# Optimization experiments

Measured on AMD Instinct MI355X. Metric: run time of the kernel, lower is better.

## Reference

```python
import jax, jax.numpy as jnp
import numpy as np

HIDDEN = 2048
INTER = 768
N_EXPERTS = 8
TOP_K = 2
BATCH, SEQ = 4, 512


def setup_inputs() -> dict:
    key = jax.random.key(0)
    ks = jax.random.split(key, 5)
    std = 0.02
    hidden_states = jax.random.normal(ks[0], (BATCH, SEQ, HIDDEN), dtype=jnp.float32)
    W_gate = jax.random.normal(ks[1], (N_EXPERTS, HIDDEN), dtype=jnp.float32) * std  # router Linear weight [E,H]
    Wg = jax.random.normal(ks[2], (N_EXPERTS, HIDDEN, INTER), dtype=jnp.float32) * std  # gate proj per expert
    Wu = jax.random.normal(ks[3], (N_EXPERTS, HIDDEN, INTER), dtype=jnp.float32) * std  # up proj per expert
    Wd = jax.random.normal(ks[4], (N_EXPERTS, INTER, HIDDEN), dtype=jnp.float32) * std  # down proj per expert
    return {"hidden_states": hidden_states, "W_gate": W_gate, "Wg": Wg, "Wu": Wu, "Wd": Wd}


def reference(hidden_states, W_gate, Wg, Wu, Wd):
    orig_shape = hidden_states.shape
    x = hidden_states.reshape(-1, HIDDEN)              # [T, H]
    T = x.shape[0]

    # Router: softmax in float32, top-k, renormalize (matches torch code).
    router_logits = x @ W_gate.T                        # [T, E]
    routing_probs = jax.nn.softmax(router_logits.astype(jnp.float32), axis=-1)
    topk_w, topk_idx = jax.lax.top_k(routing_probs, TOP_K)  # [T, K]
    topk_w = topk_w / jnp.sum(topk_w, axis=-1, keepdims=True)
    topk_w = topk_w.astype(x.dtype)

    # Sparse combine weights as dense [T, E] (equiv to index_add over torch.where dispatch).
    combine = jnp.zeros((T, N_EXPERTS), dtype=x.dtype)
    combine = combine.at[jnp.arange(T)[:, None], topk_idx].add(topk_w)

    # Expert MLPs, computed densely over experts (idiomatic jit-able dispatch).
    g = jnp.einsum('th,ehi->eti', x, Wg)                # [E, T, I]
    u = jnp.einsum('th,ehi->eti', x, Wu)                # [E, T, I]
    h = jax.nn.silu(g) * u                              # SiluAndMul
    y = jnp.einsum('eti,eih->eth', h, Wd)               # [E, T, H]

    out = jnp.einsum('eth,te->th', y, combine)          # weighted combine
    return out.reshape(orig_shape)
```

## Files before the change

### kernel.cpp

```cpp
#include <hip/hip_runtime.h>
#include <hip/hip_bf16.h>
#include <math.h>

#define H_DIM 2048
#define I_DIM 768
#define NEXP  8
#define TTOK  2048

typedef __bf16 bf16x8 __attribute__((ext_vector_type(8)));
typedef __bf16 bf16x4 __attribute__((ext_vector_type(4)));
typedef float  f32x4  __attribute__((ext_vector_type(4)));

#define WS_COUNTS   0u
#define WS_TOK      128u
#define WS_WGTW     65664u
#define WS_XBF      131328u
#define WS_HBUF     8519936u
#define WS_WG_T     15008000u
#define WS_WU_T     40173824u
#define WS_WD_T     65339648u


__device__ __forceinline__ void gl2l(const __bf16* g, __bf16* l) {
    __builtin_amdgcn_global_load_lds(
        (const __attribute__((address_space(1))) unsigned int*)g,
        (__attribute__((address_space(3))) unsigned int*)l, 16, 0, 0);
}

__device__ __forceinline__ void pipe_sync_vm8() {
    asm volatile("" ::: "memory");
    __builtin_amdgcn_s_waitcnt(0x78);
    __builtin_amdgcn_s_barrier();
    asm volatile("" ::: "memory");
}
__device__ __forceinline__ void pipe_sync_vm4() {
    asm volatile("" ::: "memory");
    __builtin_amdgcn_s_waitcnt(0x74);
    __builtin_amdgcn_s_barrier();
    asm volatile("" ::: "memory");
}
__device__ __forceinline__ void pipe_sync_vm0() {
    asm volatile("" ::: "memory");
    __builtin_amdgcn_s_waitcnt(0x70);
    __builtin_amdgcn_s_barrier();
    asm volatile("" ::: "memory");
}

#define NTRANS 18432
__global__ __launch_bounds__(128) void prep_k(
    const float* __restrict__ x, const float* __restrict__ Wgate,
    const float* __restrict__ Wg, const float* __restrict__ Wu, const float* __restrict__ Wd,
    int* __restrict__ counts, int* __restrict__ tok_list, float* __restrict__ wgt,
    __bf16* __restrict__ xb, __bf16* __restrict__ Wg_t, __bf16* __restrict__ Wu_t,
    __bf16* __restrict__ Wd_t) {
    __shared__ float sT[64 * 33];
    __shared__ float s_red[NEXP][2];
    __shared__ float s_logit[NEXP];
    const int tid = threadIdx.x;
    const int b = blockIdx.x;

    if (b >= NTRANS) {
        const int t = b - NTRANS;
        const float4* xr = (const float4*)(x + (size_t)t * H_DIM);
        bf16x4* xo = (bf16x4*)(xb + (size_t)t * H_DIM);
        float acc[NEXP];
#pragma unroll
        for (int e = 0; e < NEXP; ++e) acc[e] = 0.f;
#pragma unroll
        for (int j = 0; j < 4; ++j) {
            const int i4 = j * 128 + tid;
            float4 v = xr[i4];
            bf16x4 o;
            o[0] = (__bf16)v.x; o[1] = (__bf16)v.y; o[2] = (__bf16)v.z; o[3] = (__bf16)v.w;
            xo[i4] = o;
#pragma unroll
            for (int e = 0; e < NEXP; ++e) {
                float4 wv = *(const float4*)(Wgate + e * H_DIM + i4 * 4);
                acc[e] += v.x * wv.x + v.y * wv.y + v.z * wv.z + v.w * wv.w;
            }
        }
        const int lane = tid & 63, w = tid >> 6;
#pragma unroll
        for (int e = 0; e < NEXP; ++e) {
            float v = acc[e];
#pragma unroll
            for (int off = 32; off > 0; off >>= 1) v += __shfl_down(v, off, 64);
            if (lane == 0) s_red[e][w] = v;
        }
        __syncthreads();
        if (tid < NEXP) s_logit[tid] = s_red[tid][0] + s_red[tid][1];
        __syncthreads();
        if (tid == 0) {
            int i0 = 0; float l0 = s_logit[0];
            for (int e = 1; e < NEXP; ++e) if (s_logit[e] > l0) { l0 = s_logit[e]; i0 = e; }
            int i1 = -1; float l1 = -1e30f;
            for (int e = 0; e < NEXP; ++e) if (e != i0 && s_logit[e] > l1) { l1 = s_logit[e]; i1 = e; }
            float w0 = 1.f / (1.f + expf(l1 - l0));
            float w1 = 1.f - w0;
            int p0 = atomicAdd(&counts[i0], 1);
            tok_list[i0 * TTOK + p0] = t; wgt[i0 * TTOK + p0] = w0;
            int p1 = atomicAdd(&counts[i1], 1);
            tok_list[i1 * TTOK + p1] = t; wgt[i1 * TTOK + p1] = w1;
        }
        return;
    }

    int r = b;
    const int t3 = r / 6144; r -= t3 * 6144;
    const int e = r / 768;  const int rem = r - e * 768;
    const float* in; __bf16* out; int N, k0, n0;
    size_t tbase; int rowbase;
    if (t3 < 2) {
        N = I_DIM;
        const int kt = rem / 12, nt = rem % 12;
        k0 = kt * 32; n0 = nt * 64;
        in = t3 ? Wu : Wg; out = t3 ? Wu_t : Wg_t;
        tbase = ((size_t)(e * 12 + nt) * 64 + kt) * 2048;
        rowbase = 0;
    } else {
        N = H_DIM;
        const int kt = rem / 32, ntraw = rem % 32;
        k0 = kt * 32; n0 = ntraw * 64;
        in = Wd; out = Wd_t;
        tbase = ((size_t)(e * 16 + (ntraw >> 1)) * 24 + kt) * 4096;
        rowbase = (ntraw & 1) * 64;
    }
    const float* ip = in + (size_t)e * (N == I_DIM ? H_DIM * I_DIM : I_DIM * H_DIM);
    const int kl = tid >> 4;
    const int n4 = (tid & 15) * 4;
#pragma unroll
    for (int j = 0; j < 4; ++j) {
        int k = kl + j * 8;
        float4 v = *(const float4*)(ip + (size_t)(k0 + k) * N + n0 + n4);
        sT[(n4 + 0) * 33 + k] = v.x;
        sT[(n4 + 1) * 33 + k] = v.y;
        sT[(n4 + 2) * 33 + k] = v.z;
        sT[(n4 + 3) * 33 + k] = v.w;
    }
    __syncthreads();
    const int rn = tid >> 1;
    const int c0 = (tid & 1) * 2;
    bf16x8 o0, o1;
#pragma unroll
    for (int j = 0; j < 8; ++j) {
        o0[j] = (__bf16)sT[rn * 33 + c0 * 8 + j];
        o1[j] = (__bf16)sT[rn * 33 + c0 * 8 + 8 + j];
    }
    const int s0 = c0 ^ (rn & 3), s1 = s0 ^ 1;
    __bf16* op = out + tbase + (size_t)(rowbase + rn) * 32;
    *(bf16x8*)(op + s0 * 8) = o0;
    *(bf16x8*)(op + s1 * 8) = o1;
}

__global__ __launch_bounds__(256, 2) void gemm1_k(
    const __bf16* __restrict__ xb, const __bf16* __restrict__ Wgt,
    const __bf16* __restrict__ Wut, const int* __restrict__ counts,
    const int* __restrict__ tok_list, __bf16* __restrict__ hbuf) {
    const int g = blockIdx.x;
    const int e = g / 12, nt = g % 12;
    const int cnt = counts[e];
    const int m0 = blockIdx.y * 128;
    if (m0 >= cnt) return;
    const int tid = threadIdx.x;
    const int lane = tid & 63, w = tid >> 6;

    __shared__ __bf16 sA[4][128 * 32];
    __shared__ __bf16 sG_[4][64 * 32];
    __shared__ __bf16 sU[4][64 * 32];
    __shared__ int s_tok[128];
    __shared__ int s_off;

    if (tid == 0) { int o = 0; for (int j = 0; j < e; ++j) o += counts[j]; s_off = o; }
    if (tid < 128) {
        int m = m0 + tid;
        s_tok[tid] = tok_list[e * TTOK + (m < cnt ? m : cnt - 1)];
    }
    __syncthreads();
    const int off = s_off;

    const int srow = lane >> 2;
    const int gof = ((lane & 3) ^ (srow & 3)) * 8;
    const __bf16* pA[2]; int lofA[2];
#pragma unroll
    for (int i = 0; i < 2; ++i) {
        int r = i * 64 + w * 16 + srow;
        pA[i] = xb + (size_t)s_tok[r] * H_DIM + gof;
        lofA[i] = (i * 64 + w * 16) * 32;
    }
    const int lofGU = (w * 16) * 32;
    const __bf16* pG = Wgt + (size_t)(e * 12 + nt) * 64 * 2048 + w * 512 + lane * 8;
    const __bf16* pU = Wut + (size_t)(e * 12 + nt) * 64 * 2048 + w * 512 + lane * 8;

    const int wm = w & 1, wn = w >> 1;
    const int l15 = lane & 15, kq = lane >> 4;
    const int swz = (kq ^ (l15 & 3)) * 8;

    f32x4 accG[4][2], accU[4][2];
#pragma unroll
    for (int mf = 0; mf < 4; ++mf)
#pragma unroll
        for (int nf = 0; nf < 2; ++nf) {
            accG[mf][nf] = (f32x4){0.f, 0.f, 0.f, 0.f};
            accU[mf][nf] = (f32x4){0.f, 0.f, 0.f, 0.f};
        }

#define G1_ISSUE(T, BUF)                                             \
    {                                                                \
        gl2l(pA[0] + (T) * 32, &sA[BUF][lofA[0]]);                   \
        gl2l(pA[1] + (T) * 32, &sA[BUF][lofA[1]]);                   \
        gl2l(pG + (T) * 2048, &sG_[BUF][lofGU]);                     \
        gl2l(pU + (T) * 2048, &sU[BUF][lofGU]);                      \
    }

#define G1_COMPUTE(P)                                                                    \
    {                                                                                    \
        bf16x8 af[4], bg[2], bu[2];                                                      \
        _Pragma("unroll")                                                                \
        for (int mf = 0; mf < 4; ++mf)                                                   \
            af[mf] = *(const bf16x8*)(&sA[P][0] + (wm * 64 + mf * 16 + l15) * 32 + swz); \
        _Pragma("unroll")                                                                \
        for (int nf = 0; nf < 2; ++nf) {                                                 \
            bg[nf] = *(const bf16x8*)(&sG_[P][0] + (wn * 32 + nf * 16 + l15) * 32 + swz);\
            bu[nf] = *(const bf16x8*)(&sU[P][0] + (wn * 32 + nf * 16 + l15) * 32 + swz); \
        }                                                                                \
        _Pragma("unroll")                                                                \
        for (int mf = 0; mf < 4; ++mf)                                                   \
            _Pragma("unroll")                                                            \
            for (int nf = 0; nf < 2; ++nf) {                                             \
                accG[mf][nf] = __builtin_amdgcn_mfma_f32_16x16x32_bf16(af[mf], bg[nf], accG[mf][nf], 0, 0, 0); \
                accU[mf][nf] = __builtin_amdgcn_mfma_f32_16x16x32_bf16(af[mf], bu[nf], accU[mf][nf], 0, 0, 0); \
            }                                                                            \
    }

    G1_ISSUE(0, 0); G1_ISSUE(1, 1); G1_ISSUE(2, 2);

#pragma unroll 4
    for (int it = 0; it < 60; ++it) {
        const int p = it & 3;
        pipe_sync_vm8();
        G1_ISSUE(it + 3, (it + 3) & 3);
        G1_COMPUTE(p);
    }
    pipe_sync_vm8(); G1_ISSUE(63, 3); G1_COMPUTE(0);
    pipe_sync_vm8(); G1_COMPUTE(1);
    pipe_sync_vm4(); G1_COMPUTE(2);
    pipe_sync_vm0(); G1_COMPUTE(3);
#undef G1_ISSUE
#undef G1_COMPUTE

#pragma unroll
    for (int mf = 0; mf < 4; ++mf) {
#pragma unroll
        for (int reg = 0; reg < 4; ++reg) {
            int m = m0 + wm * 64 + mf * 16 + kq * 4 + reg;
            if (m < cnt) {
                size_t rowbase = (size_t)(off + m) * I_DIM;
#pragma unroll
                for (int nf = 0; nf < 2; ++nf) {
                    float g1 = accG[mf][nf][reg], u1 = accU[mf][nf][reg];
                    float h = (g1 / (1.f + __expf(-g1))) * u1;
                    hbuf[rowbase + nt * 64 + wn * 32 + nf * 16 + l15] = (__bf16)h;
                }
            }
        }
    }
}

__global__ __launch_bounds__(256, 2) void gemm2_k(
    const __bf16* __restrict__ hbuf, const __bf16* __restrict__ Wdt,
    const int* __restrict__ counts, const int* __restrict__ tok_list,
    const float* __restrict__ wgt, float* __restrict__ out) {
    const int g = blockIdx.x;
    const int e = g >> 4, nt = g & 15;
    const int cnt = counts[e];
    const int m0 = blockIdx.y * 128;
    if (m0 >= cnt) return;
    const int tid = threadIdx.x;
    const int lane = tid & 63, w = tid >> 6;

    __shared__ __bf16 sA[4][128 * 32];
    __shared__ __bf16 sB[4][128 * 32];
    __shared__ int s_tok[128];
    __shared__ float s_w[128];
    __shared__ int s_off;

    if (tid == 0) { int o = 0; for (int j = 0; j < e; ++j) o += counts[j]; s_off = o; }
    if (tid < 128) {
        int m = m0 + tid;
        if (m < cnt) { s_tok[tid] = tok_list[e * TTOK + m]; s_w[tid] = wgt[e * TTOK + m]; }
        else         { s_tok[tid] = 0;                      s_w[tid] = 0.f; }
    }
    __syncthreads();
    const int off = s_off;

    const int srow = lane >> 2;
    const int gof = ((lane & 3) ^ (srow & 3)) * 8;
    const __bf16* pA[2]; int lofA[2];
#pragma unroll
    for (int i = 0; i < 2; ++i) {
        int r = i * 64 + w * 16 + srow;
        pA[i] = hbuf + (size_t)(off + m0 + r) * I_DIM + gof;
        lofA[i] = (i * 64 + w * 16) * 32;
    }
    const int lofB0 = (w * 16) * 32;
    const int lofB1 = (64 + w * 16) * 32;
    const __bf16* pB0 = Wdt + (size_t)(e * 16 + nt) * 24 * 4096 + (w * 16) * 32 + lane * 8;
    const __bf16* pB1 = pB0 + 64 * 32;

    const int wm = w & 1, wn = w >> 1;
    const int l15 = lane & 15, kq = lane >> 4;
    const int swz = (kq ^ (l15 & 3)) * 8;

    f32x4 acc[4][4];
#pragma unroll
    for (int mf = 0; mf < 4; ++mf)
#pragma unroll
        for (int nf = 0; nf < 4; ++nf) acc[mf][nf] = (f32x4){0.f, 0.f, 0.f, 0.f};

#define G2_ISSUE(T, BUF)                                             \
    {                                                                \
        gl2l(pA[0] + (T) * 32, &sA[BUF][lofA[0]]);                   \
        gl2l(pA[1] + (T) * 32, &sA[BUF][lofA[1]]);                   \
        gl2l(pB0 + (T) * 4096, &sB[BUF][lofB0]);                     \
        gl2l(pB1 + (T) * 4096, &sB[BUF][lofB1]);                     \
    }

#define G2_COMPUTE(P)                                                                    \
    {                                                                                    \
        bf16x8 af[4], bb[4];                                                             \
        _Pragma("unroll")                                                                \
        for (int mf = 0; mf < 4; ++mf)                                                   \
            af[mf] = *(const bf16x8*)(&sA[P][0] + (wm * 64 + mf * 16 + l15) * 32 + swz); \
        _Pragma("unroll")                                                                \
        for (int nf = 0; nf < 4; ++nf)                                                   \
            bb[nf] = *(const bf16x8*)(&sB[P][0] + (wn * 64 + nf * 16 + l15) * 32 + swz); \
        _Pragma("unroll")                                                                \
        for (int mf = 0; mf < 4; ++mf)                                                   \
            _Pragma("unroll")                                                            \
            for (int nf = 0; nf < 4; ++nf)                                               \
                acc[mf][nf] = __builtin_amdgcn_mfma_f32_16x16x32_bf16(af[mf], bb[nf], acc[mf][nf], 0, 0, 0); \
    }

    G2_ISSUE(0, 0); G2_ISSUE(1, 1); G2_ISSUE(2, 2);
#pragma unroll 4
    for (int it = 0; it < 20; ++it) {
        const int p = it & 3;
        pipe_sync_vm8();
        G2_ISSUE(it + 3, (it + 3) & 3);
        G2_COMPUTE(p);
    }
    pipe_sync_vm8(); G2_ISSUE(23, 3); G2_COMPUTE(0);
    pipe_sync_vm8(); G2_COMPUTE(1);
    pipe_sync_vm4(); G2_COMPUTE(2);
    pipe_sync_vm0(); G2_COMPUTE(3);
#undef G2_ISSUE
#undef G2_COMPUTE

#pragma unroll
    for (int mf = 0; mf < 4; ++mf) {
#pragma unroll
        for (int reg = 0; reg < 4; ++reg) {
            int m_loc = wm * 64 + mf * 16 + kq * 4 + reg;
            if (m0 + m_loc < cnt) {
                int tok = s_tok[m_loc];
                float wv = s_w[m_loc];
                float* orow = out + (size_t)tok * H_DIM + nt * 128 + wn * 64 + l15;
#pragma unroll
                for (int nf = 0; nf < 4; ++nf)
                    atomicAdd(orow + nf * 16, wv * acc[mf][nf][reg]);
            }
        }
    }
}

extern "C" void kernel_launch(void* const* d_in, const int* in_sizes, int n_in,
                              void* d_out, int out_size, void* d_ws, size_t ws_size,
                              hipStream_t stream) {
    const float* x     = (const float*)d_in[0];
    const float* Wgate = (const float*)d_in[1];
    const float* Wg    = (const float*)d_in[2];
    const float* Wu    = (const float*)d_in[3];
    const float* Wd    = (const float*)d_in[4];
    float* out = (float*)d_out;
    char* ws = (char*)d_ws;

    int*    counts   = (int*)(ws + WS_COUNTS);
    int*    tok_list = (int*)(ws + WS_TOK);
    float*  wgt      = (float*)(ws + WS_WGTW);
    __bf16* xb       = (__bf16*)(ws + WS_XBF);
    __bf16* hbuf     = (__bf16*)(ws + WS_HBUF);
    __bf16* Wg_t     = (__bf16*)(ws + WS_WG_T);
    __bf16* Wu_t     = (__bf16*)(ws + WS_WU_T);
    __bf16* Wd_t     = (__bf16*)(ws + WS_WD_T);

    hipMemsetAsync(counts, 0, 32, stream);
    hipMemsetAsync(d_out, 0, (size_t)TTOK * H_DIM * sizeof(float), stream);

    prep_k<<<NTRANS + TTOK, 128, 0, stream>>>(x, Wgate, Wg, Wu, Wd,
                                              counts, tok_list, wgt, xb, Wg_t, Wu_t, Wd_t);
    gemm1_k<<<dim3(96, 16), 256, 0, stream>>>(xb, Wg_t, Wu_t, counts, tok_list, hbuf);
    gemm2_k<<<dim3(128, 16), 256, 0, stream>>>(hbuf, Wd_t, counts, tok_list, wgt, out);
}
```

Measured before the change: 340.4 us.

## Restructure weight transpose prep into large coalesced row-strip blocks

The weight conversion/transpose kernel now gives each 256-thread block a full 32-row strip. That strip covers all 768 columns for Wg/Wu, or 512 columns for Wd. Rows are read with fully contiguous float4 loads, converted to bf16 in shared memory, then written out as swizzled 32-wide tiles. This replaces 18432 small 128-thread blocks with 1792 larger blocks, aiming to improve DRAM read coalescing and cut per-block overhead in the memory-bound prep stage. The router blocks move to 256 threads with a 4-wave reduction; larger shared memory per block may lower occupancy.

Measured after the change: 346.8 us. No clear change (+1.9%).

```diff
diff --git a/kernel.cpp b/kernel.cpp
--- a/kernel.cpp
+++ b/kernel.cpp
@@ -46,110 +46,136 @@
     asm volatile("" ::: "memory");
 }
 
-#define NTRANS 18432
-__global__ __launch_bounds__(128) void prep_k(
+#define NBLK_A  1024
+#define NBLK_AB 1792
+__global__ __launch_bounds__(256) void prep_k(
     const float* __restrict__ x, const float* __restrict__ Wgate,
     const float* __restrict__ Wg, const float* __restrict__ Wu, const float* __restrict__ Wd,
     int* __restrict__ counts, int* __restrict__ tok_list, float* __restrict__ wgt,
     __bf16* __restrict__ xb, __bf16* __restrict__ Wg_t, __bf16* __restrict__ Wu_t,
     __bf16* __restrict__ Wd_t) {
-    __shared__ float sT[64 * 33];
-    __shared__ float s_red[NEXP][2];
+    __shared__ __bf16 sTb[32 * 772];
+    __shared__ float s_red[NEXP][4];
     __shared__ float s_logit[NEXP];
     const int tid = threadIdx.x;
     const int b = blockIdx.x;
 
-    if (b >= NTRANS) {
-        const int t = b - NTRANS;
-        const float4* xr = (const float4*)(x + (size_t)t * H_DIM);
-        bf16x4* xo = (bf16x4*)(xb + (size_t)t * H_DIM);
-        float acc[NEXP];
-#pragma unroll
-        for (int e = 0; e < NEXP; ++e) acc[e] = 0.f;
-#pragma unroll
-        for (int j = 0; j < 4; ++j) {
-            const int i4 = j * 128 + tid;
-            float4 v = xr[i4];
+    if (b < NBLK_A) {
+        const int which = b >> 9;
+        const int e = (b >> 6) & 7;
+        const int kt = b & 63;
+        const float4* ip4 = (const float4*)((which ? Wu : Wg) + ((size_t)e * H_DIM + kt * 32) * I_DIM);
+#pragma unroll
+        for (int i = 0; i < 24; ++i) {
+            const int f = i * 256 + tid;
+            const int k = f / 192;
+            const int n4 = (f - k * 192) * 4;
+            float4 v = ip4[f];
             bf16x4 o;
             o[0] = (__bf16)v.x; o[1] = (__bf16)v.y; o[2] = (__bf16)v.z; o[3] = (__bf16)v.w;
-            xo[i4] = o;
-#pragma unroll
-            for (int e = 0; e < NEXP; ++e) {
-                float4 wv = *(const float4*)(Wgate + e * H_DIM + i4 * 4);
-                acc[e] += v.x * wv.x + v.y * wv.y + v.z * wv.z + v.w * wv.w;
+            *(bf16x4*)(&sTb[k * 772 + n4]) = o;
+        }
+        __syncthreads();
+        __bf16* outp = which ? Wu_t : Wg_t;
+#pragma unroll
+        for (int i = 0; i < 3; ++i) {
+            const int n = i * 256 + tid;
+            const int nt = n >> 6, rn = n & 63;
+            __bf16 col[32];
+#pragma unroll
+            for (int k = 0; k < 32; ++k) col[k] = sTb[k * 772 + n];
+            __bf16* op = outp + ((size_t)((e * 12 + nt) * 64 + kt)) * 2048 + rn * 32;
+            const int sw = rn & 3;
+#pragma unroll
+            for (int c = 0; c < 4; ++c) {
+                bf16x8 o;
+#pragma unroll
+                for (int j = 0; j < 8; ++j) o[j] = col[c * 8 + j];
+                *(bf16x8*)(op + ((c ^ sw) * 8)) = o;
             }
         }
-        const int lane = tid & 63, w = tid >> 6;
+        return;
+    }
+
+    if (b < NBLK_AB) {
+        const int b2 = b - NBLK_A;
+        const int e = b2 / 96;
+        const int rem = b2 - e * 96;
+        const int kt = rem >> 2, q = rem & 3;
+        const float* ip = Wd + (size_t)e * I_DIM * H_DIM + (size_t)(kt * 32) * H_DIM + q * 512;
+#pragma unroll
+        for (int i = 0; i < 16; ++i) {
+            const int f = i * 256 + tid;
+            const int k = f >> 7;
+            const int n4 = (f & 127) * 4;
+            float4 v = *(const float4*)(ip + (size_t)k * H_DIM + n4);
+            bf16x4 o;
+            o[0] = (__bf16)v.x; o[1] = (__bf16)v.y; o[2] = (__bf16)v.z; o[3] = (__bf16)v.w;
+            *(bf16x4*)(&sTb[k * 516 + n4]) = o;
+        }
+        __syncthreads();
+#pragma unroll
+        for (int i = 0; i < 2; ++i) {
+            const int R = i * 256 + tid;
+            const int nt = q * 4 + (R >> 7), rn = R & 127;
+            __bf16 col[32];
+#pragma unroll
+            for (int k = 0; k < 32; ++k) col[k] = sTb[k * 516 + R];
+            __bf16* op = Wd_t + ((size_t)((e * 16 + nt) * 24 + kt)) * 4096 + rn * 32;
+            const int sw = rn & 3;
+#pragma unroll
+            for (int c = 0; c < 4; ++c) {
+                bf16x8 o;
+#pragma unroll
+                for (int j = 0; j < 8; ++j) o[j] = col[c * 8 + j];
+                *(bf16x8*)(op + ((c ^ sw) * 8)) = o;
+            }
+        }
+        return;
+    }
+
+    const int t = b - NBLK_AB;
+    const float4* xr = (const float4*)(x + (size_t)t * H_DIM);
+    bf16x4* xo = (bf16x4*)(xb + (size_t)t * H_DIM);
+    float acc[NEXP];
+#pragma unroll
+    for (int e = 0; e < NEXP; ++e) acc[e] = 0.f;
+#pragma unroll
+    for (int j = 0; j < 2; ++j) {
+        const int i4 = j * 256 + tid;
+        float4 v = xr[i4];
+        bf16x4 o;
+        o[0] = (__bf16)v.x; o[1] = (__bf16)v.y; o[2] = (__bf16)v.z; o[3] = (__bf16)v.w;
+        xo[i4] = o;
 #pragma unroll
         for (int e = 0; e < NEXP; ++e) {
-            float v = acc[e];
-#pragma unroll
-            for (int off = 32; off > 0; off >>= 1) v += __shfl_down(v, off, 64);
-            if (lane == 0) s_red[e][w] = v;
-        }
-        __syncthreads();
-        if (tid < NEXP) s_logit[tid] = s_red[tid][0] + s_red[tid][1];
-        __syncthreads();
-        if (tid == 0) {
-            int i0 = 0; float l0 = s_logit[0];
-            for (int e = 1; e < NEXP; ++e) if (s_logit[e] > l0) { l0 = s_logit[e]; i0 = e; }
-            int i1 = -1; float l1 = -1e30f;
-            for (int e = 0; e < NEXP; ++e) if (e != i0 && s_logit[e] > l1) { l1 = s_logit[e]; i1 = e; }
-            float w0 = 1.f / (1.f + expf(l1 - l0));
-            float w1 = 1.f - w0;
-            int p0 = atomicAdd(&counts[i0], 1);
-            tok_list[i0 * TTOK + p0] = t; wgt[i0 * TTOK + p0] = w0;
-            int p1 = atomicAdd(&counts[i1], 1);
-            tok_list[i1 * TTOK + p1] = t; wgt[i1 * TTOK + p1] = w1;
-        }
-        return;
-    }
-
-    int r = b;
-    const int t3 = r / 6144; r -= t3 * 6144;
-    const int e = r / 768;  const int rem = r - e * 768;
-    const float* in; __bf16* out; int N, k0, n0;
-    size_t tbase; int rowbase;
-    if (t3 < 2) {
-        N = I_DIM;
-        const int kt = rem / 12, nt = rem % 12;
-        k0 = kt * 32; n0 = nt * 64;
-        in = t3 ? Wu : Wg; out = t3 ? Wu_t : Wg_t;
-        tbase = ((size_t)(e * 12 + nt) * 64 + kt) * 2048;
-        rowbase = 0;
-    } else {
-        N = H_DIM;
-        const int kt = rem / 32, ntraw = rem % 32;
-        k0 = kt * 32; n0 = ntraw * 64;
-        in = Wd; out = Wd_t;
-        tbase = ((size_t)(e * 16 + (ntraw >> 1)) * 24 + kt) * 4096;
-        rowbase = (ntraw & 1) * 64;
-    }
-    const float* ip = in + (size_t)e * (N == I_DIM ? H_DIM * I_DIM : I_DIM * H_DIM);
-    const int kl = tid >> 4;
-    const int n4 = (tid & 15) * 4;
-#pragma unroll
-    for (int j = 0; j < 4; ++j) {
-        int k = kl + j * 8;
-        float4 v = *(const float4*)(ip + (size_t)(k0 + k) * N + n0 + n4);
-        sT[(n4 + 0) * 33 + k] = v.x;
-        sT[(n4 + 1) * 33 + k] = v.y;
-        sT[(n4 + 2) * 33 + k] = v.z;
-        sT[(n4 + 3) * 33 + k] = v.w;
+            float4 wv = *(const float4*)(Wgate + e * H_DIM + i4 * 4);
+            acc[e] += v.x * wv.x + v.y * wv.y + v.z * wv.z + v.w * wv.w;
+        }
+    }
+    const int lane = tid & 63, w = tid >> 6;
+#pragma unroll
+    for (int e = 0; e < NEXP; ++e) {
+        float v = acc[e];
+#pragma unroll
+        for (int off = 32; off > 0; off >>= 1) v += __shfl_down(v, off, 64);
+        if (lane == 0) s_red[e][w] = v;
     }
     __syncthreads();
-    const int rn = tid >> 1;
-    const int c0 = (tid & 1) * 2;
-    bf16x8 o0, o1;
-#pragma unroll
-    for (int j = 0; j < 8; ++j) {
-        o0[j] = (__bf16)sT[rn * 33 + c0 * 8 + j];
-        o1[j] = (__bf16)sT[rn * 33 + c0 * 8 + 8 + j];
-    }
-    const int s0 = c0 ^ (rn & 3), s1 = s0 ^ 1;
-    __bf16* op = out + tbase + (size_t)(rowbase + rn) * 32;
-    *(bf16x8*)(op + s0 * 8) = o0;
-    *(bf16x8*)(op + s1 * 8) = o1;
+    if (tid < NEXP) s_logit[tid] = s_red[tid][0] + s_red[tid][1] + s_red[tid][2] + s_red[tid][3];
+    __syncthreads();
+    if (tid == 0) {
+        int i0 = 0; float l0 = s_logit[0];
+        for (int e = 1; e < NEXP; ++e) if (s_logit[e] > l0) { l0 = s_logit[e]; i0 = e; }
+        int i1 = -1; float l1 = -1e30f;
+        for (int e = 0; e < NEXP; ++e) if (e != i0 && s_logit[e] > l1) { l1 = s_logit[e]; i1 = e; }
+        float w0 = 1.f / (1.f + expf(l1 - l0));
+        float w1 = 1.f - w0;
+        int p0 = atomicAdd(&counts[i0], 1);
+        tok_list[i0 * TTOK + p0] = t; wgt[i0 * TTOK + p0] = w0;
+        int p1 = atomicAdd(&counts[i1], 1);
+        tok_list[i1 * TTOK + p1] = t; wgt[i1 * TTOK + p1] = w1;
+    }
 }
 
 __global__ __launch_bounds__(256, 2) void gemm1_k(
@@ -396,8 +422,8 @@
     hipMemsetAsync(counts, 0, 32, stream);
     hipMemsetAsync(d_out, 0, (size_t)TTOK * H_DIM * sizeof(float), stream);
 
-    prep_k<<<NTRANS + TTOK, 128, 0, stream>>>(x, Wgate, Wg, Wu, Wd,
-                                              counts, tok_list, wgt, xb, Wg_t, Wu_t, Wd_t);
+    prep_k<<<NBLK_AB + TTOK, 256, 0, stream>>>(x, Wgate, Wg, Wu, Wd,
+                                               counts, tok_list, wgt, xb, Wg_t, Wu_t, Wd_t);
     gemm1_k<<<dim3(96, 16), 256, 0, stream>>>(xb, Wg_t, Wu_t, counts, tok_list, hbuf);
     gemm2_k<<<dim3(128, 16), 256, 0, stream>>>(hbuf, Wd_t, counts, tok_list, wgt, out);
 }
```

## Drop weight pre-transpose pass; stream fp32 weights into LDS and convert in GEMMs

Applied to the files above, without the earlier changes.

Removes the prep pass that transposed and converted all expert weights to bf16 every call. The GEMM kernels now load fp32 weights directly into LDS with swizzled columns and convert them to bf16 while building MFMA fragments. The software pipeline drops from 4 to 3 stages to fit the larger fp32 LDS tiles. This removes a full read/write pass over roughly 150MB of weights, at the cost of more LDS traffic, scalar LDS reads, in-loop conversion, and less latency hiding.

Result: slower. 372.5 us (+9.4%).

```diff
diff --git a/kernel.cpp b/kernel.cpp
--- a/kernel.cpp
+++ b/kernel.cpp
@@ -16,26 +16,21 @@
 #define WS_WGTW     65664u
 #define WS_XBF      131328u
 #define WS_HBUF     8519936u
-#define WS_WG_T     15008000u
-#define WS_WU_T     40173824u
-#define WS_WD_T     65339648u
-
 
 __device__ __forceinline__ void gl2l(const __bf16* g, __bf16* l) {
     __builtin_amdgcn_global_load_lds(
         (const __attribute__((address_space(1))) unsigned int*)g,
         (__attribute__((address_space(3))) unsigned int*)l, 16, 0, 0);
 }
-
-__device__ __forceinline__ void pipe_sync_vm8() {
+__device__ __forceinline__ void gl2lf(const float* g, float* l) {
+    __builtin_amdgcn_global_load_lds(
+        (const __attribute__((address_space(1))) unsigned int*)g,
+        (__attribute__((address_space(3))) unsigned int*)l, 16, 0, 0);
+}
+
+__device__ __forceinline__ void pipe_sync_vm6() {
     asm volatile("" ::: "memory");
-    __builtin_amdgcn_s_waitcnt(0x78);
-    __builtin_amdgcn_s_barrier();
-    asm volatile("" ::: "memory");
-}
-__device__ __forceinline__ void pipe_sync_vm4() {
-    asm volatile("" ::: "memory");
-    __builtin_amdgcn_s_waitcnt(0x74);
+    __builtin_amdgcn_s_waitcnt(0x76);
     __builtin_amdgcn_s_barrier();
     asm volatile("" ::: "memory");
 }
@@ -46,115 +41,60 @@
     asm volatile("" ::: "memory");
 }
 
-#define NTRANS 18432
-__global__ __launch_bounds__(128) void prep_k(
+__global__ __launch_bounds__(256) void router_k(
     const float* __restrict__ x, const float* __restrict__ Wgate,
-    const float* __restrict__ Wg, const float* __restrict__ Wu, const float* __restrict__ Wd,
     int* __restrict__ counts, int* __restrict__ tok_list, float* __restrict__ wgt,
-    __bf16* __restrict__ xb, __bf16* __restrict__ Wg_t, __bf16* __restrict__ Wu_t,
-    __bf16* __restrict__ Wd_t) {
-    __shared__ float sT[64 * 33];
-    __shared__ float s_red[NEXP][2];
+    __bf16* __restrict__ xb) {
+    __shared__ float s_red[NEXP][4];
     __shared__ float s_logit[NEXP];
     const int tid = threadIdx.x;
-    const int b = blockIdx.x;
-
-    if (b >= NTRANS) {
-        const int t = b - NTRANS;
-        const float4* xr = (const float4*)(x + (size_t)t * H_DIM);
-        bf16x4* xo = (bf16x4*)(xb + (size_t)t * H_DIM);
-        float acc[NEXP];
-#pragma unroll
-        for (int e = 0; e < NEXP; ++e) acc[e] = 0.f;
-#pragma unroll
-        for (int j = 0; j < 4; ++j) {
-            const int i4 = j * 128 + tid;
-            float4 v = xr[i4];
-            bf16x4 o;
-            o[0] = (__bf16)v.x; o[1] = (__bf16)v.y; o[2] = (__bf16)v.z; o[3] = (__bf16)v.w;
-            xo[i4] = o;
-#pragma unroll
-            for (int e = 0; e < NEXP; ++e) {
-                float4 wv = *(const float4*)(Wgate + e * H_DIM + i4 * 4);
-                acc[e] += v.x * wv.x + v.y * wv.y + v.z * wv.z + v.w * wv.w;
-            }
+    const int t = blockIdx.x;
+    const float4* xr = (const float4*)(x + (size_t)t * H_DIM);
+    bf16x4* xo = (bf16x4*)(xb + (size_t)t * H_DIM);
+    float acc[NEXP];
+#pragma unroll
+    for (int e = 0; e < NEXP; ++e) acc[e] = 0.f;
+#pragma unroll
+    for (int j = 0; j < 2; ++j) {
+        const int i4 = j * 256 + tid;
+        float4 v = xr[i4];
+        bf16x4 o;
+        o[0] = (__bf16)v.x; o[1] = (__bf16)v.y; o[2] = (__bf16)v.z; o[3] = (__bf16)v.w;
+        xo[i4] = o;
+#pragma unroll
+        for (int e = 0; e < NEXP; ++e) {
+            float4 wv = *(const float4*)(Wgate + e * H_DIM + i4 * 4);
+            acc[e] += v.x * wv.x + v.y * wv.y + v.z * wv.z + v.w * wv.w;
         }
-        const int lane = tid & 63, w = tid >> 6;
-#pragma unroll
-        for (int e = 0; e < NEXP; ++e) {
-            float v = acc[e];
-#pragma unroll
-            for (int off = 32; off > 0; off >>= 1) v += __shfl_down(v, off, 64);
-            if (lane == 0) s_red[e][w] = v;
-        }
-        __syncthreads();
-        if (tid < NEXP) s_logit[tid] = s_red[tid][0] + s_red[tid][1];
-        __syncthreads();
-        if (tid == 0) {
-            int i0 = 0; float l0 = s_logit[0];
-            for (int e = 1; e < NEXP; ++e) if (s_logit[e] > l0) { l0 = s_logit[e]; i0 = e; }
-            int i1 = -1; float l1 = -1e30f;
-            for (int e = 0; e < NEXP; ++e) if (e != i0 && s_logit[e] > l1) { l1 = s_logit[e]; i1 = e; }
-            float w0 = 1.f / (1.f + expf(l1 - l0));
-            float w1 = 1.f - w0;
-            int p0 = atomicAdd(&counts[i0], 1);
-            tok_list[i0 * TTOK + p0] = t; wgt[i0 * TTOK + p0] = w0;
-            int p1 = atomicAdd(&counts[i1], 1);
-            tok_list[i1 * TTOK + p1] = t; wgt[i1 * TTOK + p1] = w1;
-        }
-        return;
-    }
-
-    int r = b;
-    const int t3 = r / 6144; r -= t3 * 6144;
-    const int e = r / 768;  const int rem = r - e * 768;
-    const float* in; __bf16* out; int N, k0, n0;
-    size_t tbase; int rowbase;
-    if (t3 < 2) {
-        N = I_DIM;
-        const int kt = rem / 12, nt = rem % 12;
-        k0 = kt * 32; n0 = nt * 64;
-        in = t3 ? Wu : Wg; out = t3 ? Wu_t : Wg_t;
-        tbase = ((size_t)(e * 12 + nt) * 64 + kt) * 2048;
-        rowbase = 0;
-    } else {
-        N = H_DIM;
-        const int kt = rem / 32, ntraw = rem % 32;
-        k0 = kt * 32; n0 = ntraw * 64;
-        in = Wd; out = Wd_t;
-        tbase = ((size_t)(e * 16 + (ntraw >> 1)) * 24 + kt) * 4096;
-        rowbase = (ntraw & 1) * 64;
-    }
-    const float* ip = in + (size_t)e * (N == I_DIM ? H_DIM * I_DIM : I_DIM * H_DIM);
-    const int kl = tid >> 4;
-    const int n4 = (tid & 15) * 4;
-#pragma unroll
-    for (int j = 0; j < 4; ++j) {
-        int k = kl + j * 8;
-        float4 v = *(const float4*)(ip + (size_t)(k0 + k) * N + n0 + n4);
-        sT[(n4 + 0) * 33 + k] = v.x;
-        sT[(n4 + 1) * 33 + k] = v.y;
-        sT[(n4 + 2) * 33 + k] = v.z;
-        sT[(n4 + 3) * 33 + k] = v.w;
+    }
+    const int lane = tid & 63, w = tid >> 6;
+#pragma unroll
+    for (int e = 0; e < NEXP; ++e) {
+        float v = acc[e];
+#pragma unroll
+        for (int off = 32; off > 0; off >>= 1) v += __shfl_down(v, off, 64);
+        if (lane == 0) s_red[e][w] = v;
     }
     __syncthreads();
-    const int rn = tid >> 1;
-    const int c0 = (tid & 1) * 2;
-    bf16x8 o0, o1;
-#pragma unroll
-    for (int j = 0; j < 8; ++j) {
-        o0[j] = (__bf16)sT[rn * 33 + c0 * 8 + j];
-        o1[j] = (__bf16)sT[rn * 33 + c0 * 8 + 8 + j];
-    }
-    const int s0 = c0 ^ (rn & 3), s1 = s0 ^ 1;
-    __bf16* op = out + tbase + (size_t)(rowbase + rn) * 32;
-    *(bf16x8*)(op + s0 * 8) = o0;
-    *(bf16x8*)(op + s1 * 8) = o1;
+    if (tid < NEXP) s_logit[tid] = s_red[tid][0] + s_red[tid][1] + s_red[tid][2] + s_red[tid][3];
+    __syncthreads();
+    if (tid == 0) {
+        int i0 = 0; float l0 = s_logit[0];
+        for (int e = 1; e < NEXP; ++e) if (s_logit[e] > l0) { l0 = s_logit[e]; i0 = e; }
+        int i1 = -1; float l1 = -1e30f;
+        for (int e = 0; e < NEXP; ++e) if (e != i0 && s_logit[e] > l1) { l1 = s_logit[e]; i1 = e; }
+        float w0 = 1.f / (1.f + expf(l1 - l0));
+        float w1 = 1.f - w0;
+        int p0 = atomicAdd(&counts[i0], 1);
+        tok_list[i0 * TTOK + p0] = t; wgt[i0 * TTOK + p0] = w0;
+        int p1 = atomicAdd(&counts[i1], 1);
+        tok_list[i1 * TTOK + p1] = t; wgt[i1 * TTOK + p1] = w1;
+    }
 }
 
 __global__ __launch_bounds__(256, 2) void gemm1_k(
-    const __bf16* __restrict__ xb, const __bf16* __restrict__ Wgt,
-    const __bf16* __restrict__ Wut, const int* __restrict__ counts,
+    const __bf16* __restrict__ xb, const float* __restrict__ Wg,
+    const float* __restrict__ Wu, const int* __restrict__ counts,
     const int* __restrict__ tok_list, __bf16* __restrict__ hbuf) {
     const int g = blockIdx.x;
     const int e = g / 12, nt = g % 12;
@@ -164,9 +104,9 @@
     const int tid = threadIdx.x;
     const int lane = tid & 63, w = tid >> 6;
 
-    __shared__ __bf16 sA[4][128 * 32];
-    __shared__ __bf16 sG_[4][64 * 32];
-    __shared__ __bf16 sU[4][64 * 32];
+    __shared__ __bf16 sA[3][128 * 32];
+    __shared__ float  sGf[3][32 * 64];
+    __shared__ float  sUf[3][32 * 64];
     __shared__ int s_tok[128];
     __shared__ int s_off;
 
@@ -187,13 +127,16 @@
         pA[i] = xb + (size_t)s_tok[r] * H_DIM + gof;
         lofA[i] = (i * 64 + w * 16) * 32;
     }
-    const int lofGU = (w * 16) * 32;
-    const __bf16* pG = Wgt + (size_t)(e * 12 + nt) * 64 * 2048 + w * 512 + lane * 8;
-    const __bf16* pU = Wut + (size_t)(e * 12 + nt) * 64 * 2048 + w * 512 + lane * 8;
+    const int bcol = ((lane & 15) * 4) ^ ((w & 1) * 16);
+    const float* pGf = Wg + (size_t)e * H_DIM * I_DIM + (size_t)(w * 8 + (lane >> 4)) * I_DIM + nt * 64 + bcol;
+    const float* pUf = Wu + (size_t)e * H_DIM * I_DIM + (size_t)(w * 8 + (lane >> 4)) * I_DIM + nt * 64 + bcol;
+    const int lofB0 = (w * 8) * 64;
+    const int lofB1 = (w * 8 + 4) * 64;
 
     const int wm = w & 1, wn = w >> 1;
     const int l15 = lane & 15, kq = lane >> 4;
     const int swz = (kq ^ (l15 & 3)) * 8;
+    const int xw = (kq & 1) * 16;
 
     f32x4 accG[4][2], accU[4][2];
 #pragma unroll
@@ -204,12 +147,15 @@
             accU[mf][nf] = (f32x4){0.f, 0.f, 0.f, 0.f};
         }
 
-#define G1_ISSUE(T, BUF)                                             \
-    {                                                                \
-        gl2l(pA[0] + (T) * 32, &sA[BUF][lofA[0]]);                   \
-        gl2l(pA[1] + (T) * 32, &sA[BUF][lofA[1]]);                   \
-        gl2l(pG + (T) * 2048, &sG_[BUF][lofGU]);                     \
-        gl2l(pU + (T) * 2048, &sU[BUF][lofGU]);                      \
+#define G1_ISSUE(T, BUF)                                                   \
+    {                                                                      \
+        const size_t ks_ = (size_t)(T) * 32 * I_DIM;                       \
+        gl2l(pA[0] + (T) * 32, &sA[BUF][lofA[0]]);                         \
+        gl2l(pA[1] + (T) * 32, &sA[BUF][lofA[1]]);                         \
+        gl2lf(pGf + ks_,             &sGf[BUF][lofB0]);                    \
+        gl2lf(pGf + ks_ + 4 * I_DIM, &sGf[BUF][lofB1]);                    \
+        gl2lf(pUf + ks_,             &sUf[BUF][lofB0]);                    \
+        gl2lf(pUf + ks_ + 4 * I_DIM, &sUf[BUF][lofB1]);                    \
     }
 
 #define G1_COMPUTE(P)                                                                    \
@@ -220,8 +166,12 @@
             af[mf] = *(const bf16x8*)(&sA[P][0] + (wm * 64 + mf * 16 + l15) * 32 + swz); \
         _Pragma("unroll")                                                                \
         for (int nf = 0; nf < 2; ++nf) {                                                 \
-            bg[nf] = *(const bf16x8*)(&sG_[P][0] + (wn * 32 + nf * 16 + l15) * 32 + swz);\
-            bu[nf] = *(const bf16x8*)(&sU[P][0] + (wn * 32 + nf * 16 + l15) * 32 + swz); \
+            const int nc_ = ((wn * 32 + nf * 16 + l15) ^ xw) + kq * 8 * 64;              \
+            _Pragma("unroll")                                                            \
+            for (int j = 0; j < 8; ++j) {                                                \
+                bg[nf][j] = (__bf16)sGf[P][nc_ + j * 64];                                \
+                bu[nf][j] = (__bf16)sUf[P][nc_ + j * 64];                                \
+            }                                                                            \
         }                                                                                \
         _Pragma("unroll")                                                                \
         for (int mf = 0; mf < 4; ++mf)                                                   \
@@ -232,19 +182,17 @@
             }                                                                            \
     }
 
-    G1_ISSUE(0, 0); G1_ISSUE(1, 1); G1_ISSUE(2, 2);
-
-#pragma unroll 4
-    for (int it = 0; it < 60; ++it) {
-        const int p = it & 3;
-        pipe_sync_vm8();
-        G1_ISSUE(it + 3, (it + 3) & 3);
+    G1_ISSUE(0, 0); G1_ISSUE(1, 1);
+    int p = 0, q = 2;
+    for (int it = 0; it < 62; ++it) {
+        pipe_sync_vm6();
+        G1_ISSUE(it + 2, q);
         G1_COMPUTE(p);
-    }
-    pipe_sync_vm8(); G1_ISSUE(63, 3); G1_COMPUTE(0);
-    pipe_sync_vm8(); G1_COMPUTE(1);
-    pipe_sync_vm4(); G1_COMPUTE(2);
-    pipe_sync_vm0(); G1_COMPUTE(3);
+        p = (p == 2) ? 0 : p + 1;
+        q = (q == 2) ? 0 : q + 1;
+    }
+    pipe_sync_vm6(); G1_COMPUTE(2);
+    pipe_sync_vm0(); G1_COMPUTE(0);
 #undef G1_ISSUE
 #undef G1_COMPUTE
 
@@ -267,7 +215,7 @@
 }
 
 __global__ __launch_bounds__(256, 2) void gemm2_k(
-    const __bf16* __restrict__ hbuf, const __bf16* __restrict__ Wdt,
+    const __bf16* __restrict__ hbuf, const float* __restrict__ Wd,
     const int* __restrict__ counts, const int* __restrict__ tok_list,
     const float* __restrict__ wgt, float* __restrict__ out) {
     const int g = blockIdx.x;
@@ -278,8 +226,8 @@
     const int tid = threadIdx.x;
     const int lane = tid & 63, w = tid >> 6;
 
-    __shared__ __bf16 sA[4][128 * 32];
-    __shared__ __bf16 sB[4][128 * 32];
+    __shared__ __bf16 sA[3][128 * 32];
+    __shared__ float  sBf[3][32 * 128];
     __shared__ int s_tok[128];
     __shared__ float s_w[128];
     __shared__ int s_off;
@@ -302,14 +250,14 @@
         pA[i] = hbuf + (size_t)(off + m0 + r) * I_DIM + gof;
         lofA[i] = (i * 64 + w * 16) * 32;
     }
-    const int lofB0 = (w * 16) * 32;
-    const int lofB1 = (64 + w * 16) * 32;
-    const __bf16* pB0 = Wdt + (size_t)(e * 16 + nt) * 24 * 4096 + (w * 16) * 32 + lane * 8;
-    const __bf16* pB1 = pB0 + 64 * 32;
+    const int bcol = ((lane & 31) * 4) ^ ((w & 1) * 16);
+    const float* pBf = Wd + (size_t)e * I_DIM * H_DIM + (size_t)(w * 8 + (lane >> 5)) * H_DIM + nt * 128 + bcol;
+    const int lofB = (w * 8) * 128;
 
     const int wm = w & 1, wn = w >> 1;
     const int l15 = lane & 15, kq = lane >> 4;
     const int swz = (kq ^ (l15 & 3)) * 8;
+    const int xw = (kq & 1) * 16;
 
     f32x4 acc[4][4];
 #pragma unroll
@@ -317,12 +265,15 @@
 #pragma unroll
         for (int nf = 0; nf < 4; ++nf) acc[mf][nf] = (f32x4){0.f, 0.f, 0.f, 0.f};
 
-#define G2_ISSUE(T, BUF)                                             \
-    {                                                                \
-        gl2l(pA[0] + (T) * 32, &sA[BUF][lofA[0]]);                   \
-        gl2l(pA[1] + (T) * 32, &sA[BUF][lofA[1]]);                   \
-        gl2l(pB0 + (T) * 4096, &sB[BUF][lofB0]);                     \
-        gl2l(pB1 + (T) * 4096, &sB[BUF][lofB1]);                     \
+#define G2_ISSUE(T, BUF)                                                   \
+    {                                                                      \
+        const size_t ks_ = (size_t)(T) * 32 * H_DIM;                       \
+        gl2l(pA[0] + (T) * 32, &sA[BUF][lofA[0]]);                         \
+        gl2l(pA[1] + (T) * 32, &sA[BUF][lofA[1]]);                         \
+        gl2lf(pBf + ks_,             &sBf[BUF][lofB]);                     \
+        gl2lf(pBf + ks_ + 2 * H_DIM, &sBf[BUF][lofB + 2 * 128]);           \
+        gl2lf(pBf + ks_ + 4 * H_DIM, &sBf[BUF][lofB + 4 * 128]);           \
+        gl2lf(pBf + ks_ + 6 * H_DIM, &sBf[BUF][lofB + 6 * 128]);           \
     }
 
 #define G2_COMPUTE(P)                                                                    \
@@ -332,8 +283,11 @@
         for (int mf = 0; mf < 4; ++mf)                                                   \
             af[mf] = *(const bf16x8*)(&sA[P][0] + (wm * 64 + mf * 16 + l15) * 32 + swz); \
         _Pragma("unroll")                                                                \
-        for (int nf = 0; nf < 4; ++nf)                                                   \
-            bb[nf] = *(const bf16x8*)(&sB[P][0] + (wn * 64 + nf * 16 + l15) * 32 + swz); \
+        for (int nf = 0; nf < 4; ++nf) {                                                 \
+            const int nc_ = ((wn * 64 + nf * 16 + l15) ^ xw) + kq * 8 * 128;             \
+            _Pragma("unroll")                                                            \
+            for (int j = 0; j < 8; ++j) bb[nf][j] = (__bf16)sBf[P][nc_ + j * 128];       \
+        }                                                                                \
         _Pragma("unroll")                                                                \
         for (int mf = 0; mf < 4; ++mf)                                                   \
             _Pragma("unroll")                                                            \
@@ -341,18 +295,17 @@
                 acc[mf][nf] = __builtin_amdgcn_mfma_f32_16x16x32_bf16(af[mf], bb[nf], acc[mf][nf], 0, 0, 0); \
     }
 
-    G2_ISSUE(0, 0); G2_ISSUE(1, 1); G2_ISSUE(2, 2);
-#pragma unroll 4
-    for (int it = 0; it < 20; ++it) {
-        const int p = it & 3;
-        pipe_sync_vm8();
-        G2_ISSUE(it + 3, (it + 3) & 3);
+    G2_ISSUE(0, 0); G2_ISSUE(1, 1);
+    int p = 0, q = 2;
+    for (int it = 0; it < 22; ++it) {
+        pipe_sync_vm6();
+        G2_ISSUE(it + 2, q);
         G2_COMPUTE(p);
-    }
-    pipe_sync_vm8(); G2_ISSUE(23, 3); G2_COMPUTE(0);
-    pipe_sync_vm8(); G2_COMPUTE(1);
-    pipe_sync_vm4(); G2_COMPUTE(2);
-    pipe_sync_vm0(); G2_COMPUTE(3);
+        p = (p == 2) ? 0 : p + 1;
+        q = (q == 2) ? 0 : q + 1;
+    }
+    pipe_sync_vm6(); G2_COMPUTE(1);
+    pipe_sync_vm0(); G2_COMPUTE(2);
 #undef G2_ISSUE
 #undef G2_COMPUTE
 
@@ -389,15 +342,11 @@
     float*  wgt      = (float*)(ws + WS_WGTW);
     __bf16* xb       = (__bf16*)(ws + WS_XBF);
     __bf16* hbuf     = (__bf16*)(ws + WS_HBUF);
-    __bf16* Wg_t     = (__bf16*)(ws + WS_WG_T);
-    __bf16* Wu_t     = (__bf16*)(ws + WS_WU_T);
-    __bf16* Wd_t     = (__bf16*)(ws + WS_WD_T);
 
     hipMemsetAsync(counts, 0, 32, stream);
     hipMemsetAsync(d_out, 0, (size_t)TTOK * H_DIM * sizeof(float), stream);
 
-    prep_k<<<NTRANS + TTOK, 128, 0, stream>>>(x, Wgate, Wg, Wu, Wd,
-                                              counts, tok_list, wgt, xb, Wg_t, Wu_t, Wd_t);
-    gemm1_k<<<dim3(96, 16), 256, 0, stream>>>(xb, Wg_t, Wu_t, counts, tok_list, hbuf);
-    gemm2_k<<<dim3(128, 16), 256, 0, stream>>>(hbuf, Wd_t, counts, tok_list, wgt, out);
-}
+    router_k<<<TTOK, 256, 0, stream>>>(x, Wgate, counts, tok_list, wgt, xb);
+    gemm1_k<<<dim3(96, 16), 256, 0, stream>>>(xb, Wg, Wu, counts, tok_list, hbuf);
+    gemm2_k<<<dim3(128, 16), 256, 0, stream>>>(hbuf, Wd, counts, tok_list, wgt, out);
+}
```
